# Kernel optimization log

Measured on AMD Instinct MI355X. Metric: run time of the kernel, lower is better.

Reference implementation:

```python
import jax, jax.numpy as jnp
import numpy as np

SEQ, IN, HID = 8192, 1024, 1024

def setup_inputs() -> dict:
    key = jax.random.key(0)
    k0, k1, k2, k3, k4 = jax.random.split(key, 5)
    s = 1.0 / np.sqrt(HID)  # PyTorch GRU default init scale
    return {
        "inp":  jax.random.normal(k0, (SEQ, IN), jnp.float32),
        "W_ih": jax.random.uniform(k1, (3 * HID, IN), jnp.float32, -s, s),
        "W_hh": jax.random.uniform(k2, (3 * HID, HID), jnp.float32, -s, s),
        "b_ih": jax.random.uniform(k3, (3 * HID,), jnp.float32, -s, s),
        "b_hh": jax.random.uniform(k4, (3 * HID,), jnp.float32, -s, s),
    }

def reference(inp, W_ih, W_hh, b_ih, b_hh):
    # Precompute input-side gate projections for all timesteps in one GEMM: [S, 3H]
    gx = inp @ W_ih.T + b_ih
    h0 = jnp.zeros((HID,), inp.dtype)

    def step(h, gx_t):
        gh = W_hh @ h + b_hh           # [3H]
        xr, xz, xn = jnp.split(gx_t, 3)
        hr, hz, hn = jnp.split(gh, 3)
        r = jax.nn.sigmoid(xr + hr)
        z = jax.nn.sigmoid(xz + hz)
        n = jnp.tanh(xn + r * hn)      # PyTorch GRU: r gates the hidden candidate term
        h_new = (1.0 - z) * n + z * h
        return h_new, h_new

    _, outs = jax.lax.scan(step, h0, gx)  # outs: [S, H], matches torch loop output
    return outs
```

## Files before the change

### kernel.cpp

```cpp
#include <hip/hip_runtime.h>

#define SEQ  8192
#define HID  1024
#define NBLK 64
#define WPB  16
#define TPB  (WPB * 64)
#define KCH  (HID / 64)

#define SLOT_WORDS (2 * HID)

__device__ __forceinline__ float sigmoidf_fast(float a) {
    return 1.0f / (1.0f + __expf(-a));
}
__device__ __forceinline__ float tanhf_fast(float a) {
    float t = fabsf(a);
    float e = __expf(-2.0f * t);
    float r = (1.0f - e) / (1.0f + e);
    return copysignf(r, a);
}

__global__ __launch_bounds__(TPB, 4) void gru_persistent(
    const float* __restrict__ inp,
    const float* __restrict__ Wih,
    const float* __restrict__ Whh,
    const float* __restrict__ bih,
    const float* __restrict__ bhh,
    float* __restrict__ out,
    unsigned long long* __restrict__ slots)
{
    __shared__ float h_lds[HID];
    const int tid  = threadIdx.x;
    const int wave = tid >> 6;
    const int lane = tid & 63;
    const int j    = blockIdx.x * WPB + wave;

    float wr[KCH], wz[KCH], wn[KCH];
    {
        const float* Wr = Whh + (size_t)j * HID;
        const float* Wz = Whh + (size_t)(HID + j) * HID;
        const float* Wn = Whh + (size_t)(2 * HID + j) * HID;
#pragma unroll
        for (int k = 0; k < KCH; ++k) {
            wr[k] = Wr[lane + 64 * k];
            wz[k] = Wz[lane + 64 * k];
            wn[k] = Wn[lane + 64 * k];
        }
    }
    const float bxr = bih[j], bxz = bih[HID + j], bxn = bih[2 * HID + j];
    const float bhr = bhh[j], bhz = bhh[HID + j], bhn = bhh[2 * HID + j];
    const float* Ur = Wih + (size_t)j * HID;
    const float* Uz = Wih + (size_t)(HID + j) * HID;
    const float* Un = Wih + (size_t)(2 * HID + j) * HID;

    float xr = 0.0f, xz = 0.0f, xn = 0.0f;
    {
        const float* x = inp;
#pragma unroll
        for (int k = 0; k < KCH; ++k) {
            float xv = x[lane + 64 * k];
            xr = fmaf(Ur[lane + 64 * k], xv, xr);
            xz = fmaf(Uz[lane + 64 * k], xv, xz);
            xn = fmaf(Un[lane + 64 * k], xv, xn);
        }
#pragma unroll
        for (int m = 32; m >= 1; m >>= 1) {
            xr += __shfl_xor(xr, m, 64);
            xz += __shfl_xor(xz, m, 64);
            xn += __shfl_xor(xn, m, 64);
        }
        xr += bxr; xz += bxz; xn += bxn;
    }

    for (int t = 1; t <= SEQ; ++t) {
        unsigned long long* rd = slots + ((t - 1) & 1) * HID;
        if (wave == 0) {
            const unsigned expect = (unsigned)(t - 1);
            for (;;) {
                float v[KCH];
                bool ok = true;
#pragma unroll
                for (int k = 0; k < KCH; ++k) {
                    unsigned long long wv = __hip_atomic_load(
                        rd + lane + 64 * k, __ATOMIC_RELAXED, __HIP_MEMORY_SCOPE_AGENT);
                    ok &= ((unsigned)(wv >> 32) == expect);
                    v[k] = __uint_as_float((unsigned)(wv & 0xffffffffu));
                }
                if (__all(ok)) {
#pragma unroll
                    for (int k = 0; k < KCH; ++k) h_lds[lane + 64 * k] = v[k];
                    break;
                }
                __builtin_amdgcn_s_sleep(1);
            }
        }
        __syncthreads();

        float hr = 0.0f, hz = 0.0f, hn = 0.0f;
#pragma unroll
        for (int k = 0; k < KCH; ++k) {
            float hv = h_lds[lane + 64 * k];
            hr = fmaf(wr[k], hv, hr);
            hz = fmaf(wz[k], hv, hz);
            hn = fmaf(wn[k], hv, hn);
        }
#pragma unroll
        for (int m = 32; m >= 1; m >>= 1) {
            hr += __shfl_xor(hr, m, 64);
            hz += __shfl_xor(hz, m, 64);
            hn += __shfl_xor(hn, m, 64);
        }
        hr += bhr; hz += bhz; hn += bhn;

        const float hprev = h_lds[j];
        const float r = sigmoidf_fast(xr + hr);
        const float z = sigmoidf_fast(xz + hz);
        const float n = tanhf_fast(xn + r * hn);
        const float hnew = (1.0f - z) * n + z * hprev;

        if (lane == 0) {
            unsigned long long pub = ((unsigned long long)(unsigned)t << 32)
                                   | (unsigned long long)__float_as_uint(hnew);
            __hip_atomic_store(slots + (t & 1) * HID + j, pub,
                               __ATOMIC_RELAXED, __HIP_MEMORY_SCOPE_AGENT);
            __builtin_nontemporal_store(hnew, out + (size_t)(t - 1) * HID + j);
        }

        if (t < SEQ) {
            const float* x = inp + (size_t)t * HID;
            xr = 0.0f; xz = 0.0f; xn = 0.0f;
#pragma unroll
            for (int k = 0; k < KCH; ++k) {
                float xv = x[lane + 64 * k];
                xr = fmaf(Ur[lane + 64 * k], xv, xr);
                xz = fmaf(Uz[lane + 64 * k], xv, xz);
                xn = fmaf(Un[lane + 64 * k], xv, xn);
            }
#pragma unroll
            for (int m = 32; m >= 1; m >>= 1) {
                xr += __shfl_xor(xr, m, 64);
                xz += __shfl_xor(xz, m, 64);
                xn += __shfl_xor(xn, m, 64);
            }
            xr += bxr; xz += bxz; xn += bxn;
        }
    }
}

extern "C" void kernel_launch(void* const* d_in, const int* in_sizes, int n_in,
                              void* d_out, int out_size, void* d_ws, size_t ws_size,
                              hipStream_t stream) {
    const float* inp = (const float*)d_in[0];
    const float* Wih = (const float*)d_in[1];
    const float* Whh = (const float*)d_in[2];
    const float* bih = (const float*)d_in[3];
    const float* bhh = (const float*)d_in[4];
    float* out = (float*)d_out;
    unsigned long long* slots = (unsigned long long*)d_ws;

    hipMemsetAsync(slots, 0, SLOT_WORDS * sizeof(unsigned long long), stream);

    gru_persistent<<<dim3(NBLK), dim3(TPB), 0, stream>>>(
        inp, Wih, Whh, bih, bhh, out, slots);
}
```

Before: 59.15 ms.

## Spread hidden-state polling across all waves with double-buffered LDS

Every wave now polls one 64-element slice of the published hidden state, instead of wave 0 polling all 1024 values alone. The hidden state moves into a double-buffered LDS array, so the next step's buffer can be filled while the current one is still being read, and there is one barrier per step. Polling starts after the input-projection work for the next step, so that GEMV is overlapped with waiting on the other blocks. The cost is 16 waves issuing atomic polls at once, which adds L2 traffic.

```diff
diff --git a/kernel.cpp b/kernel.cpp
--- a/kernel.cpp
+++ b/kernel.cpp
@@ -28,11 +28,12 @@
     float* __restrict__ out,
     unsigned long long* __restrict__ slots)
 {
-    __shared__ float h_lds[HID];
+    __shared__ float hbuf[2][HID];
     const int tid  = threadIdx.x;
     const int wave = tid >> 6;
     const int lane = tid & 63;
     const int j    = blockIdx.x * WPB + wave;
+    const int sl   = (wave << 6) | lane;
 
     float wr[KCH], wz[KCH], wn[KCH];
     {
@@ -51,6 +52,9 @@
     const float* Ur = Wih + (size_t)j * HID;
     const float* Uz = Wih + (size_t)(HID + j) * HID;
     const float* Un = Wih + (size_t)(2 * HID + j) * HID;
+
+    hbuf[0][tid] = 0.0f;
+    __syncthreads();
 
     float xr = 0.0f, xz = 0.0f, xn = 0.0f;
     {
@@ -72,33 +76,11 @@
     }
 
     for (int t = 1; t <= SEQ; ++t) {
-        unsigned long long* rd = slots + ((t - 1) & 1) * HID;
-        if (wave == 0) {
-            const unsigned expect = (unsigned)(t - 1);
-            for (;;) {
-                float v[KCH];
-                bool ok = true;
-#pragma unroll
-                for (int k = 0; k < KCH; ++k) {
-                    unsigned long long wv = __hip_atomic_load(
-                        rd + lane + 64 * k, __ATOMIC_RELAXED, __HIP_MEMORY_SCOPE_AGENT);
-                    ok &= ((unsigned)(wv >> 32) == expect);
-                    v[k] = __uint_as_float((unsigned)(wv & 0xffffffffu));
-                }
-                if (__all(ok)) {
-#pragma unroll
-                    for (int k = 0; k < KCH; ++k) h_lds[lane + 64 * k] = v[k];
-                    break;
-                }
-                __builtin_amdgcn_s_sleep(1);
-            }
-        }
-        __syncthreads();
-
+        const float* hb = hbuf[(t - 1) & 1];
         float hr = 0.0f, hz = 0.0f, hn = 0.0f;
 #pragma unroll
         for (int k = 0; k < KCH; ++k) {
-            float hv = h_lds[lane + 64 * k];
+            float hv = hb[lane + 64 * k];
             hr = fmaf(wr[k], hv, hr);
             hz = fmaf(wz[k], hv, hz);
             hn = fmaf(wn[k], hv, hn);
@@ -111,7 +93,7 @@
         }
         hr += bhr; hz += bhz; hn += bhn;
 
-        const float hprev = h_lds[j];
+        const float hprev = hb[j];
         const float r = sigmoidf_fast(xr + hr);
         const float z = sigmoidf_fast(xz + hz);
         const float n = tanhf_fast(xn + r * hn);
@@ -126,23 +108,38 @@
         }
 
         if (t < SEQ) {
-            const float* x = inp + (size_t)t * HID;
-            xr = 0.0f; xz = 0.0f; xn = 0.0f;
+            {
+                const float* x = inp + (size_t)t * HID;
+                xr = 0.0f; xz = 0.0f; xn = 0.0f;
 #pragma unroll
-            for (int k = 0; k < KCH; ++k) {
-                float xv = x[lane + 64 * k];
-                xr = fmaf(Ur[lane + 64 * k], xv, xr);
-                xz = fmaf(Uz[lane + 64 * k], xv, xz);
-                xn = fmaf(Un[lane + 64 * k], xv, xn);
+                for (int k = 0; k < KCH; ++k) {
+                    float xv = x[lane + 64 * k];
+                    xr = fmaf(Ur[lane + 64 * k], xv, xr);
+                    xz = fmaf(Uz[lane + 64 * k], xv, xz);
+                    xn = fmaf(Un[lane + 64 * k], xv, xn);
+                }
+#pragma unroll
+                for (int m = 32; m >= 1; m >>= 1) {
+                    xr += __shfl_xor(xr, m, 64);
+                    xz += __shfl_xor(xz, m, 64);
+                    xn += __shfl_xor(xn, m, 64);
+                }
+                xr += bxr; xz += bxz; xn += bxn;
             }
-#pragma unroll
-            for (int m = 32; m >= 1; m >>= 1) {
-                xr += __shfl_xor(xr, m, 64);
-                xz += __shfl_xor(xz, m, 64);
-                xn += __shfl_xor(xn, m, 64);
+
+            const unsigned long long* rd = slots + (t & 1) * HID;
+            const unsigned expect = (unsigned)t;
+            for (;;) {
+                unsigned long long wv = __hip_atomic_load(
+                    rd + sl, __ATOMIC_RELAXED, __HIP_MEMORY_SCOPE_AGENT);
+                if (__all((unsigned)(wv >> 32) == expect)) {
+                    hbuf[t & 1][sl] = __uint_as_float((unsigned)(wv & 0xffffffffu));
+                    break;
+                }
+                __builtin_amdgcn_s_sleep(1);
             }
-            xr += bxr; xz += bxz; xn += bxn;
         }
+        __syncthreads();
     }
 }
 
```

After: 68.31 ms. +15.5%, slower.

## Offload wave 0 input projection to wave 1 and poll slots per-chunk with backoff

Applied to the files above, without the earlier changes.

The polling wave (wave 0) no longer computes its own input-side projection after publishing. Wave 1 computes it for the next step and passes it through a double-buffered LDS slot, so wave 0 can return to polling sooner. The poll loop now re-reads only the chunks that are still pending and uses longer sleeps after a few iterations, and the biases for the r and z gates are folded together. The cost is that wave 1 does twice the input-projection work each step, which may lengthen the step if wave 1 ends up on the critical path.

```diff
diff --git a/kernel.cpp b/kernel.cpp
--- a/kernel.cpp
+++ b/kernel.cpp
@@ -4,9 +4,8 @@
 #define HID  1024
 #define NBLK 64
 #define WPB  16
-#define TPB  (WPB * 64)
-#define KCH  (HID / 64)
-
+#define TPB  1024
+#define KCH  16
 #define SLOT_WORDS (2 * HID)
 
 __device__ __forceinline__ float sigmoidf_fast(float a) {
@@ -19,6 +18,30 @@
     return copysignf(r, a);
 }
 
+__device__ __forceinline__ void dot3(const float* __restrict__ x,
+                                     const float* __restrict__ pr,
+                                     const float* __restrict__ pz,
+                                     const float* __restrict__ pn,
+                                     int lane, float& dr, float& dz, float& dn)
+{
+    float ar = 0.f, az = 0.f, an = 0.f;
+#pragma unroll
+    for (int k = 0; k < KCH; ++k) {
+        const int i = lane + 64 * k;
+        float xv = x[i];
+        ar = fmaf(pr[i], xv, ar);
+        az = fmaf(pz[i], xv, az);
+        an = fmaf(pn[i], xv, an);
+    }
+#pragma unroll
+    for (int m = 32; m >= 1; m >>= 1) {
+        ar += __shfl_xor(ar, m, 64);
+        az += __shfl_xor(az, m, 64);
+        an += __shfl_xor(an, m, 64);
+    }
+    dr = ar; dz = az; dn = an;
+}
+
 __global__ __launch_bounds__(TPB, 4) void gru_persistent(
     const float* __restrict__ inp,
     const float* __restrict__ Wih,
@@ -28,7 +51,8 @@
     float* __restrict__ out,
     unsigned long long* __restrict__ slots)
 {
-    __shared__ float h_lds[HID];
+    __shared__ float hbuf[HID];
+    __shared__ float xh[2][4];
     const int tid  = threadIdx.x;
     const int wave = tid >> 6;
     const int lane = tid & 63;
@@ -46,59 +70,63 @@
             wn[k] = Wn[lane + 64 * k];
         }
     }
-    const float bxr = bih[j], bxz = bih[HID + j], bxn = bih[2 * HID + j];
-    const float bhr = bhh[j], bhz = bhh[HID + j], bhn = bhh[2 * HID + j];
+    const float bra  = bih[j]           + bhh[j];
+    const float bza  = bih[HID + j]     + bhh[HID + j];
+    const float bxn  = bih[2 * HID + j];
+    const float bhn  = bhh[2 * HID + j];
+
     const float* Ur = Wih + (size_t)j * HID;
     const float* Uz = Wih + (size_t)(HID + j) * HID;
     const float* Un = Wih + (size_t)(2 * HID + j) * HID;
 
-    float xr = 0.0f, xz = 0.0f, xn = 0.0f;
-    {
-        const float* x = inp;
-#pragma unroll
-        for (int k = 0; k < KCH; ++k) {
-            float xv = x[lane + 64 * k];
-            xr = fmaf(Ur[lane + 64 * k], xv, xr);
-            xz = fmaf(Uz[lane + 64 * k], xv, xz);
-            xn = fmaf(Un[lane + 64 * k], xv, xn);
+    float xdr = 0.f, xdz = 0.f, xdn = 0.f;
+    if (wave != 0) {
+        dot3(inp, Ur, Uz, Un, lane, xdr, xdz, xdn);
+        if (wave == 1) {
+            float pr, pz, pn;
+            dot3(inp, Ur - HID, Uz - HID, Un - HID, lane, pr, pz, pn);
+            if (lane == 0) { xh[1][0] = pr; xh[1][1] = pz; xh[1][2] = pn; }
         }
-#pragma unroll
-        for (int m = 32; m >= 1; m >>= 1) {
-            xr += __shfl_xor(xr, m, 64);
-            xz += __shfl_xor(xz, m, 64);
-            xn += __shfl_xor(xn, m, 64);
-        }
-        xr += bxr; xz += bxz; xn += bxn;
     }
 
     for (int t = 1; t <= SEQ; ++t) {
-        unsigned long long* rd = slots + ((t - 1) & 1) * HID;
         if (wave == 0) {
+            const unsigned long long* rd = slots + ((t - 1) & 1) * HID;
             const unsigned expect = (unsigned)(t - 1);
+            float v[KCH];
+            bool pend[KCH];
+#pragma unroll
+            for (int k = 0; k < KCH; ++k) pend[k] = true;
+            int iter = 0;
             for (;;) {
-                float v[KCH];
-                bool ok = true;
+                bool anypend = false;
 #pragma unroll
                 for (int k = 0; k < KCH; ++k) {
-                    unsigned long long wv = __hip_atomic_load(
-                        rd + lane + 64 * k, __ATOMIC_RELAXED, __HIP_MEMORY_SCOPE_AGENT);
-                    ok &= ((unsigned)(wv >> 32) == expect);
-                    v[k] = __uint_as_float((unsigned)(wv & 0xffffffffu));
+                    if (pend[k]) {
+                        unsigned long long wv = __hip_atomic_load(
+                            rd + lane + 64 * k, __ATOMIC_RELAXED, __HIP_MEMORY_SCOPE_AGENT);
+                        if ((unsigned)(wv >> 32) == expect) {
+                            v[k] = __uint_as_float((unsigned)(wv & 0xffffffffu));
+                            pend[k] = false;
+                        } else {
+                            anypend = true;
+                        }
+                    }
                 }
-                if (__all(ok)) {
+                if (__all(!anypend)) break;
+                if (iter < 2) __builtin_amdgcn_s_sleep(1);
+                else          __builtin_amdgcn_s_sleep(8);
+                ++iter;
+            }
 #pragma unroll
-                    for (int k = 0; k < KCH; ++k) h_lds[lane + 64 * k] = v[k];
-                    break;
-                }
-                __builtin_amdgcn_s_sleep(1);
-            }
+            for (int k = 0; k < KCH; ++k) hbuf[lane + 64 * k] = v[k];
         }
         __syncthreads();
 
-        float hr = 0.0f, hz = 0.0f, hn = 0.0f;
+        float hr = 0.f, hz = 0.f, hn = 0.f;
 #pragma unroll
         for (int k = 0; k < KCH; ++k) {
-            float hv = h_lds[lane + 64 * k];
+            float hv = hbuf[lane + 64 * k];
             hr = fmaf(wr[k], hv, hr);
             hz = fmaf(wz[k], hv, hz);
             hn = fmaf(wn[k], hv, hn);
@@ -109,39 +137,40 @@
             hz += __shfl_xor(hz, m, 64);
             hn += __shfl_xor(hn, m, 64);
         }
-        hr += bhr; hz += bhz; hn += bhn;
 
-        const float hprev = h_lds[j];
-        const float r = sigmoidf_fast(xr + hr);
-        const float z = sigmoidf_fast(xz + hz);
-        const float n = tanhf_fast(xn + r * hn);
+        float xr = xdr, xz = xdz, xn = xdn;
+        if (wave == 0) {
+            const float* xp = xh[t & 1];
+            xr = xp[0]; xz = xp[1]; xn = xp[2];
+        }
+
+        const float hprev = hbuf[j];
+        const float r = sigmoidf_fast(xr + hr + bra);
+        const float z = sigmoidf_fast(xz + hz + bza);
+        const float n = tanhf_fast(xn + bxn + r * (hn + bhn));
         const float hnew = (1.0f - z) * n + z * hprev;
 
         if (lane == 0) {
-            unsigned long long pub = ((unsigned long long)(unsigned)t << 32)
-                                   | (unsigned long long)__float_as_uint(hnew);
-            __hip_atomic_store(slots + (t & 1) * HID + j, pub,
-                               __ATOMIC_RELAXED, __HIP_MEMORY_SCOPE_AGENT);
+            if (t < SEQ) {
+                unsigned long long pub = ((unsigned long long)(unsigned)t << 32)
+                                       | (unsigned long long)__float_as_uint(hnew);
+                __hip_atomic_store(slots + (t & 1) * HID + j, pub,
+                                   __ATOMIC_RELAXED, __HIP_MEMORY_SCOPE_AGENT);
+            }
             __builtin_nontemporal_store(hnew, out + (size_t)(t - 1) * HID + j);
         }
 
-        if (t < SEQ) {
+        if (t < SEQ && wave != 0) {
             const float* x = inp + (size_t)t * HID;
-            xr = 0.0f; xz = 0.0f; xn = 0.0f;
-#pragma unroll
-            for (int k = 0; k < KCH; ++k) {
-                float xv = x[lane + 64 * k];
-                xr = fmaf(Ur[lane + 64 * k], xv, xr);
-                xz = fmaf(Uz[lane + 64 * k], xv, xz);
-                xn = fmaf(Un[lane + 64 * k], xv, xn);
+            dot3(x, Ur, Uz, Un, lane, xdr, xdz, xdn);
+            if (wave == 1) {
+                float pr, pz, pn;
+                dot3(x, Ur - HID, Uz - HID, Un - HID, lane, pr, pz, pn);
+                if (lane == 0) {
+                    float* xp = xh[(t + 1) & 1];
+                    xp[0] = pr; xp[1] = pz; xp[2] = pn;
+                }
             }
-#pragma unroll
-            for (int m = 32; m >= 1; m >>= 1) {
-                xr += __shfl_xor(xr, m, 64);
-                xz += __shfl_xor(xz, m, 64);
-                xn += __shfl_xor(xn, m, 64);
-            }
-            xr += bxr; xz += bxz; xn += bxn;
         }
     }
 }
```

Result: slower. 99.99 ms (+69.0%).
